# Optimization experiments

Hardware: AMD Instinct MI355X
Metric: run time of the kernel (lower is better)

## Reference

```python
import jax, jax.numpy as jnp
import numpy as np

B, N, C, H = 4, 1024, 768, 12
D = C // H
SCALE = D ** -0.5


def setup_inputs() -> dict:
    key = jax.random.key(0)
    k1, k2, k3, k4 = jax.random.split(key, 4)
    x1 = jax.random.normal(k1, (B, N, C), dtype=jnp.float32)
    x2 = jax.random.normal(k2, (B, N, C), dtype=jnp.float32)
    # shared (dual-stream) Linear2 weights, torch nn.Linear layout: [out, in]
    W_qkv = jax.random.normal(k3, (3 * C, C), dtype=jnp.float32) * (C ** -0.5)
    b_qkv = jnp.zeros((3 * C,), dtype=jnp.float32)
    W_proj = jax.random.normal(k4, (C, C), dtype=jnp.float32) * (C ** -0.5)
    b_proj = jnp.zeros((C,), dtype=jnp.float32)
    return {"x1": x1, "x2": x2, "W_qkv": W_qkv, "b_qkv": b_qkv,
            "W_proj": W_proj, "b_proj": b_proj}


def _split_qkv(x, W_qkv, b_qkv):
    qkv = (x @ W_qkv.T + b_qkv).reshape(B, N, 3, H, D)
    qkv = jnp.transpose(qkv, (2, 0, 3, 1, 4))  # [3,B,H,N,D]
    return qkv[0], qkv[1], qkv[2]


def reference(x1, x2, W_qkv, b_qkv, W_proj, b_proj):
    q1, k1, v1 = _split_qkv(x1, W_qkv, b_qkv)
    q2, k2, v2 = _split_qkv(x2, W_qkv, b_qkv)
    # two score maps, combined before a single shared softmax
    s1 = jnp.einsum("bhqd,bhkd->bhqk", q1 * SCALE, k1)
    s2 = jnp.einsum("bhqd,bhkd->bhqk", q2 * SCALE, k2)
    attn = jax.nn.softmax(s1 + s2, axis=-1)  # [B,H,N,N]
    # same attention matrix applied to both value streams
    o1 = jnp.einsum("bhqk,bhkd->bhqd", attn, v1)
    o2 = jnpum = jnp.einsum("bhqk,bhkd->bhqd", attn, v2) if False else jnp.einsum("bhqk,bhkd->bhqd", attn, v2)
    o1 = jnp.transpose(o1, (0, 2, 1, 3)).reshape(B, N, C)
    o2 = jnp.transpose(o2, (0, 2, 1, 3)).reshape(B, N, C)
    y1 = o1 @ W_proj.T + b_proj
    y2 = o2 @ W_proj.T + b_proj
    return y1, y2
```

## Files before the change

### kernel.cpp

```cpp
#include <hip/hip_runtime.h>
#include <hip/hip_bf16.h>


typedef __bf16 bf16x8 __attribute__((ext_vector_type(8)));
typedef __bf16 bf16x4 __attribute__((ext_vector_type(4)));
typedef float  f32x4  __attribute__((ext_vector_type(4)));

__device__ __forceinline__ bf16x8 cvt8(const float* p) {
    f32x4 f0 = *(const f32x4*)p;
    f32x4 f1 = *(const f32x4*)(p + 4);
    bf16x8 r;
    r[0] = (__bf16)f0[0]; r[1] = (__bf16)f0[1]; r[2] = (__bf16)f0[2]; r[3] = (__bf16)f0[3];
    r[4] = (__bf16)f1[0]; r[5] = (__bf16)f1[1]; r[6] = (__bf16)f1[2]; r[7] = (__bf16)f1[3];
    return r;
}

__device__ __forceinline__ void async16(const __bf16* g, __bf16* l) {
    __builtin_amdgcn_global_load_lds(
        (const __attribute__((address_space(1))) void*)g,
        (__attribute__((address_space(3))) void*)l, 16, 0, 0);
}

__global__ __launch_bounds__(256)
void cvt3_k(const float* __restrict__ x1, const float* __restrict__ x2,
            const float* __restrict__ wq, __bf16* __restrict__ xc,
            __bf16* __restrict__ wqc)
{
    int bid = blockIdx.x;
    const float* src; __bf16* dst; int i;
    if (bid < 1536)      { src = x1; dst = xc;             i = (bid * 256 + threadIdx.x) * 8; }
    else if (bid < 3072) { src = x2; dst = xc + 3145728;   i = ((bid - 1536) * 256 + threadIdx.x) * 8; }
    else                 { src = wq; dst = wqc;            i = ((bid - 3072) * 256 + threadIdx.x) * 8; }
    *(bf16x8*)(dst + i) = cvt8(src + i);
}

__global__ __launch_bounds__(256)
void cvt_k(const float* __restrict__ src, __bf16* __restrict__ dst, int n) {
    int i = (blockIdx.x * 256 + threadIdx.x) * 8;
    if (i < n) *(bf16x8*)(dst + i) = cvt8(src + i);
}

__global__ __launch_bounds__(256)
void gemm_qkv_s(const __bf16* __restrict__ Xc, const __bf16* __restrict__ Wq,
                const float* __restrict__ bias,
                __bf16* __restrict__ qo, __bf16* __restrict__ ko,
                __bf16* __restrict__ vo)
{
    constexpr int K = 768;
    __shared__ __bf16 As[128 * 32];
    __shared__ __bf16 Bs[128 * 32];

    const int t = threadIdx.x, w = t >> 6, lane = t & 63;
    const int l15 = lane & 15, quad = lane >> 4;
    const int wm = w >> 1, wn = w & 1;

    const int bid  = blockIdx.x;
    const int xcd  = bid & 7;
    const int i6   = bid >> 3;
    const int pair = i6 / 18;
    const int gx   = i6 - pair * 18;
    const int p    = xcd * 8 + pair;
    const int gy   = p & 31;
    const int st   = p >> 5;

    const int lrow = lane >> 2, lcol = (lane & 3) * 8;

    const __bf16* Ab = Xc + (size_t)st * 3145728 + (size_t)(gy * 128) * K;
    const __bf16* Bb = Wq + (size_t)(gx * 128) * K;

    f32x4 acc[4][4];
#pragma unroll
    for (int mi = 0; mi < 4; mi++)
#pragma unroll
        for (int ni = 0; ni < 4; ni++) acc[mi][ni] = f32x4{0.f, 0.f, 0.f, 0.f};

    for (int k0 = 0; k0 < K; k0 += 32) {
#pragma unroll
        for (int i = 0; i < 2; i++) {
            int r = w * 32 + i * 16 + lrow;
            async16(Ab + (size_t)r * K + k0 + lcol, &As[r * 32 + lcol]);
            async16(Bb + (size_t)r * K + k0 + lcol, &Bs[r * 32 + lcol]);
        }
        __syncthreads();
        bf16x8 af[4], bfr[4];
#pragma unroll
        for (int mi = 0; mi < 4; mi++)
            af[mi] = *(const bf16x8*)&As[(wm * 64 + mi * 16 + l15) * 32 + quad * 8];
#pragma unroll
        for (int ni = 0; ni < 4; ni++)
            bfr[ni] = *(const bf16x8*)&Bs[(wn * 64 + ni * 16 + l15) * 32 + quad * 8];
#pragma unroll
        for (int mi = 0; mi < 4; mi++)
#pragma unroll
            for (int ni = 0; ni < 4; ni++)
                acc[mi][ni] = __builtin_amdgcn_mfma_f32_16x16x32_bf16(af[mi], bfr[ni], acc[mi][ni], 0, 0, 0);
        __syncthreads();
    }

    const int which = (gx * 128) / 768;

    if (which == 2) {
#pragma unroll
        for (int ni = 0; ni < 4; ni++) {
            int j = gx * 128 + wn * 64 + ni * 16 + l15;
            int c = j - 1536;
            int h = c >> 6, d = c & 63;
            float bj = bias[j];
#pragma unroll
            for (int mi = 0; mi < 4; mi++) {
                int row0 = gy * 128 + wm * 64 + mi * 16 + quad * 4;
                int b = row0 >> 10, tok0 = row0 & 1023;
                bf16x4 pv;
#pragma unroll
                for (int r = 0; r < 4; r++) pv[r] = (__bf16)(acc[mi][ni][r] + bj);
                *(bf16x4*)&vo[((size_t)((st * 4 + b) * 12 + h) * 64 + d) * 1024 + tok0] = pv;
            }
        }
    } else {
#pragma unroll
        for (int ni = 0; ni < 4; ni++) {
            int j     = gx * 128 + wn * 64 + ni * 16 + l15;
            int c     = j - which * 768;
            int h = c >> 6, d = c & 63;
            float bj  = bias[j];
#pragma unroll
            for (int mi = 0; mi < 4; mi++) {
#pragma unroll
                for (int r = 0; r < 4; r++) {
                    int row = gy * 128 + wm * 64 + mi * 16 + quad * 4 + r;
                    int b = row >> 10, tok = row & 1023;
                    float val = acc[mi][ni][r] + bj;
                    if (which == 0)
                        qo[((size_t)((st * 4 + b) * 12 + h) * 1024 + tok) * 64 + d] = (__bf16)(val * 0.125f);
                    else
                        ko[((size_t)((st * 4 + b) * 12 + h) * 1024 + tok) * 64 + d] = (__bf16)val;
                }
            }
        }
    }
}

__global__ __launch_bounds__(256)
void gemm_proj(const __bf16* __restrict__ A, const __bf16* __restrict__ Wp,
               const float* __restrict__ bias, float* __restrict__ out)
{
    constexpr int K = 768;
    __shared__ __bf16 As[128 * 32];
    __shared__ __bf16 Bs[128 * 32];

    const int t = threadIdx.x, w = t >> 6, lane = t & 63;
    const int l15 = lane & 15, quad = lane >> 4;
    const int wm = w >> 1, wn = w & 1;
    const int gx = blockIdx.x, gy = blockIdx.y;
    const int lrow = lane >> 2, lcol = (lane & 3) * 8;

    const __bf16* Ab = A  + (size_t)(gy * 128) * K;
    const __bf16* Bb = Wp + (size_t)(gx * 128) * K;

    f32x4 acc[4][4];
#pragma unroll
    for (int mi = 0; mi < 4; mi++)
#pragma unroll
        for (int ni = 0; ni < 4; ni++) acc[mi][ni] = f32x4{0.f, 0.f, 0.f, 0.f};

    for (int k0 = 0; k0 < K; k0 += 32) {
#pragma unroll
        for (int i = 0; i < 2; i++) {
            int r = w * 32 + i * 16 + lrow;
            async16(Ab + (size_t)r * K + k0 + lcol, &As[r * 32 + lcol]);
            async16(Bb + (size_t)r * K + k0 + lcol, &Bs[r * 32 + lcol]);
        }
        __syncthreads();
        bf16x8 af[4], bfr[4];
#pragma unroll
        for (int mi = 0; mi < 4; mi++)
            af[mi] = *(const bf16x8*)&As[(wm * 64 + mi * 16 + l15) * 32 + quad * 8];
#pragma unroll
        for (int ni = 0; ni < 4; ni++)
            bfr[ni] = *(const bf16x8*)&Bs[(wn * 64 + ni * 16 + l15) * 32 + quad * 8];
#pragma unroll
        for (int mi = 0; mi < 4; mi++)
#pragma unroll
            for (int ni = 0; ni < 4; ni++)
                acc[mi][ni] = __builtin_amdgcn_mfma_f32_16x16x32_bf16(af[mi], bfr[ni], acc[mi][ni], 0, 0, 0);
        __syncthreads();
    }

#pragma unroll
    for (int ni = 0; ni < 4; ni++) {
        int col  = gx * 128 + wn * 64 + ni * 16 + l15;
        float bj = bias[col];
#pragma unroll
        for (int mi = 0; mi < 4; mi++)
#pragma unroll
            for (int r = 0; r < 4; r++) {
                int row = gy * 128 + wm * 64 + mi * 16 + quad * 4 + r;
                out[(size_t)row * 768 + col] = acc[mi][ni][r] + bj;
            }
    }
}

__global__ __launch_bounds__(256)
void attn_k(const __bf16* __restrict__ qws, const __bf16* __restrict__ kws,
            const __bf16* __restrict__ vws, __bf16* __restrict__ ows)
{
    __shared__ __bf16 KV[2][2][2][2][4][512];
    __shared__ __bf16 Ps[4][16 * 72];

    const int g  = blockIdx.x;
    const int qt = g / 48;
    const int bh = g % 48;
    const int b = bh / 12, h = bh % 12;
    const int t = threadIdx.x, w = t >> 6, lane = t & 63;
    const int l15 = lane & 15, quad = lane >> 4;

    const size_t head_off = (size_t)bh * 65536;
    const size_t ss       = (size_t)48 * 65536;

    bf16x8 qf[2][2];
#pragma unroll
    for (int s = 0; s < 2; s++)
#pragma unroll
        for (int kk = 0; kk < 2; kk++)
            qf[s][kk] = *(const bf16x8*)(qws + s * ss + head_off
                          + (size_t)(qt * 64 + w * 16 + l15) * 64 + kk * 32 + quad * 8);

    float lsum = 0.f;
    f32x4 accO[2][4];
#pragma unroll
    for (int s = 0; s < 2; s++)
#pragma unroll
        for (int mi = 0; mi < 4; mi++) accO[s][mi] = f32x4{0.f, 0.f, 0.f, 0.f};

    const int skv = w >> 1, sst = w & 1;
    const __bf16* sbase = (skv ? vws : kws) + head_off + (size_t)sst * ss;

#pragma unroll
    for (int i = 0; i < 8; i++) {
        const int kk = i >> 2, mi = i & 3;
        const __bf16* gp = skv
            ? sbase + (size_t)(mi * 16 + l15) * 1024 + kk * 32 + quad * 8
            : sbase + (size_t)(mi * 16 + l15) * 64 + kk * 32 + quad * 8;
        async16(gp, &KV[0][skv][sst][kk][mi][lane * 8]);
    }
    __syncthreads();

#pragma unroll 2
    for (int kt = 0; kt < 16; kt++) {
        const int cb = kt & 1, nb = cb ^ 1;

        if (kt < 15) {
            const int keyb = (kt + 1) * 64;
#pragma unroll
            for (int i = 0; i < 8; i++) {
                const int kk = i >> 2, mi = i & 3;
                const __bf16* gp = skv
                    ? sbase + (size_t)(mi * 16 + l15) * 1024 + keyb + kk * 32 + quad * 8
                    : sbase + (size_t)(keyb + mi * 16 + l15) * 64 + kk * 32 + quad * 8;
                async16(gp, &KV[nb][skv][sst][kk][mi][lane * 8]);
            }
        }

        f32x4 accS[4];
#pragma unroll
        for (int i = 0; i < 4; i++) accS[i] = f32x4{0.f, 0.f, 0.f, 0.f};
        __builtin_amdgcn_s_setprio(1);
#pragma unroll
        for (int s = 0; s < 2; s++)
#pragma unroll
            for (int kk = 0; kk < 2; kk++) {
                bf16x8 kf[4];
#pragma unroll
                for (int mi = 0; mi < 4; mi++)
                    kf[mi] = *(const bf16x8*)&KV[cb][0][s][kk][mi][lane * 8];
#pragma unroll
                for (int mi = 0; mi < 4; mi++)
                    accS[mi] = __builtin_amdgcn_mfma_f32_16x16x32_bf16(kf[mi], qf[s][kk], accS[mi], 0, 0, 0);
            }
        __builtin_amdgcn_s_setprio(0);

        float rs = 0.f;
        bf16x4 pk[4];
#pragma unroll
        for (int mi = 0; mi < 4; mi++)
#pragma unroll
            for (int r = 0; r < 4; r++) {
                float pv = __expf(accS[mi][r]);
                pk[mi][r] = (__bf16)pv;
                rs += pv;
            }
        lsum += rs;

#pragma unroll
        for (int mi = 0; mi < 4; mi++)
            *(bf16x4*)&Ps[w][l15 * 72 + mi * 16 + quad * 4] = pk[mi];

        __builtin_amdgcn_s_setprio(1);
#pragma unroll
        for (int kk = 0; kk < 2; kk++) {
            bf16x8 pa = *(const bf16x8*)&Ps[w][l15 * 72 + kk * 32 + quad * 8];
#pragma unroll
            for (int s = 0; s < 2; s++)
#pragma unroll
                for (int mi = 0; mi < 4; mi++) {
                    bf16x8 vf = *(const bf16x8*)&KV[cb][1][s][kk][mi][lane * 8];
                    accO[s][mi] = __builtin_amdgcn_mfma_f32_16x16x32_bf16(vf, pa, accO[s][mi], 0, 0, 0);
                }
        }
        __builtin_amdgcn_s_setprio(0);

        __syncthreads();
    }

    lsum += __shfl_xor(lsum, 16);
    lsum += __shfl_xor(lsum, 32);
    float il = 1.f / lsum;

    const int tok = qt * 64 + w * 16 + l15;
#pragma unroll
    for (int s = 0; s < 2; s++)
#pragma unroll
        for (int mi = 0; mi < 4; mi++) {
            bf16x4 ov;
#pragma unroll
            for (int r = 0; r < 4; r++) ov[r] = (__bf16)(accO[s][mi][r] * il);
            *(bf16x4*)&ows[((size_t)((s * 4 + b) * 1024 + tok)) * 768
                           + h * 64 + mi * 16 + quad * 4] = ov;
        }
}

extern "C" void kernel_launch(void* const* d_in, const int* in_sizes, int n_in,
                              void* d_out, int out_size, void* d_ws, size_t ws_size,
                              hipStream_t stream)
{
    const float* x1    = (const float*)d_in[0];
    const float* x2    = (const float*)d_in[1];
    const float* Wqkv  = (const float*)d_in[2];
    const float* bqkv  = (const float*)d_in[3];
    const float* Wproj = (const float*)d_in[4];
    const float* bproj = (const float*)d_in[5];
    float* out = (float*)d_out;

    const size_t qkv_elems = (size_t)2 * 4 * 12 * 1024 * 64;
    __bf16* q_ws = (__bf16*)d_ws;
    __bf16* k_ws = q_ws + qkv_elems;
    __bf16* v_ws = k_ws + qkv_elems;
    __bf16* pool = v_ws + qkv_elems;
    __bf16* Wqc  = pool + 3145728;
    __bf16* o_ws = pool;
    __bf16* Wpc  = q_ws;
    __bf16* Xc   = (__bf16*)d_out;

    cvt3_k<<<3936, 256, 0, stream>>>(x1, x2, Wqkv, Xc, Wqc);
    gemm_qkv_s<<<1152, 256, 0, stream>>>(Xc, Wqc, bqkv, q_ws, k_ws, v_ws);
    attn_k<<<768, 256, 0, stream>>>(q_ws, k_ws, v_ws, o_ws);
    cvt_k<<<288, 256, 0, stream>>>(Wproj, Wpc, 589824);
    gemm_proj<<<dim3(6, 64), 256, 0, stream>>>(o_ws, Wpc, bproj, out);
}
```

Measured before the change: 228.3 us.

## Restructure attention to two waves each handling 32 queries with smaller key tiles

New measurement: 219.1 us. 1.04x faster.

```diff
diff --git a/kernel.cpp b/kernel.cpp
--- a/kernel.cpp
+++ b/kernel.cpp
@@ -200,12 +200,13 @@
     }
 }
 
-__global__ __launch_bounds__(256)
+__global__ __launch_bounds__(128, 2)
 void attn_k(const __bf16* __restrict__ qws, const __bf16* __restrict__ kws,
             const __bf16* __restrict__ vws, __bf16* __restrict__ ows)
 {
-    __shared__ __bf16 KV[2][2][2][2][4][512];
-    __shared__ __bf16 Ps[4][16 * 72];
+    __shared__ __bf16 Ks[2][2][2][2][512];
+    __shared__ __bf16 Vs[2][2][4][512];
+    __shared__ __bf16 Ps[2][2][16 * 72];
 
     const int g  = blockIdx.x;
     const int qt = g / 48;
@@ -217,116 +218,131 @@
     const size_t head_off = (size_t)bh * 65536;
     const size_t ss       = (size_t)48 * 65536;
 
-    bf16x8 qf[2][2];
-#pragma unroll
-    for (int s = 0; s < 2; s++)
-#pragma unroll
-        for (int kk = 0; kk < 2; kk++)
-            qf[s][kk] = *(const bf16x8*)(qws + s * ss + head_off
-                          + (size_t)(qt * 64 + w * 16 + l15) * 64 + kk * 32 + quad * 8);
-
-    float lsum = 0.f;
-    f32x4 accO[2][4];
-#pragma unroll
-    for (int s = 0; s < 2; s++)
-#pragma unroll
-        for (int mi = 0; mi < 4; mi++) accO[s][mi] = f32x4{0.f, 0.f, 0.f, 0.f};
-
-    const int skv = w >> 1, sst = w & 1;
-    const __bf16* sbase = (skv ? vws : kws) + head_off + (size_t)sst * ss;
-
-#pragma unroll
-    for (int i = 0; i < 8; i++) {
-        const int kk = i >> 2, mi = i & 3;
-        const __bf16* gp = skv
-            ? sbase + (size_t)(mi * 16 + l15) * 1024 + kk * 32 + quad * 8
-            : sbase + (size_t)(mi * 16 + l15) * 64 + kk * 32 + quad * 8;
-        async16(gp, &KV[0][skv][sst][kk][mi][lane * 8]);
-    }
+    bf16x8 qf[2][2][2];
+#pragma unroll
+    for (int set = 0; set < 2; set++)
+#pragma unroll
+        for (int s = 0; s < 2; s++)
+#pragma unroll
+            for (int kk = 0; kk < 2; kk++)
+                qf[set][s][kk] = *(const bf16x8*)(qws + s * ss + head_off
+                    + (size_t)(qt * 64 + w * 32 + set * 16 + l15) * 64 + kk * 32 + quad * 8);
+
+    float lsum[2] = {0.f, 0.f};
+    f32x4 accO[2][2][4];
+#pragma unroll
+    for (int set = 0; set < 2; set++)
+#pragma unroll
+        for (int s = 0; s < 2; s++)
+#pragma unroll
+            for (int mi = 0; mi < 4; mi++) accO[set][s][mi] = f32x4{0.f, 0.f, 0.f, 0.f};
+
+    const __bf16* kbase = kws + head_off;
+    const __bf16* vbase = vws + head_off;
+
+#define STAGE_TILE(BUF, KEYB)                                                   \
+    do {                                                                        \
+        if (w == 0) {                                                           \
+            _Pragma("unroll")                                                   \
+            for (int i = 0; i < 8; i++) {                                       \
+                const int s = i >> 2, kk = (i >> 1) & 1, mi = i & 1;            \
+                async16(kbase + s * ss + (size_t)((KEYB) + mi * 16 + l15) * 64  \
+                            + kk * 32 + quad * 8,                               \
+                        &Ks[BUF][s][kk][mi][lane * 8]);                         \
+            }                                                                   \
+        } else {                                                                \
+            _Pragma("unroll")                                                   \
+            for (int i = 0; i < 8; i++) {                                       \
+                const int s = i >> 2, mi = i & 3;                               \
+                async16(vbase + s * ss + (size_t)(mi * 16 + l15) * 1024         \
+                            + (KEYB) + quad * 8,                                \
+                        &Vs[BUF][s][mi][lane * 8]);                             \
+            }                                                                   \
+        }                                                                       \
+    } while (0)
+
+    STAGE_TILE(0, 0);
     __syncthreads();
 
 #pragma unroll 2
-    for (int kt = 0; kt < 16; kt++) {
+    for (int kt = 0; kt < 32; kt++) {
         const int cb = kt & 1, nb = cb ^ 1;
 
-        if (kt < 15) {
-            const int keyb = (kt + 1) * 64;
-#pragma unroll
-            for (int i = 0; i < 8; i++) {
-                const int kk = i >> 2, mi = i & 3;
-                const __bf16* gp = skv
-                    ? sbase + (size_t)(mi * 16 + l15) * 1024 + keyb + kk * 32 + quad * 8
-                    : sbase + (size_t)(keyb + mi * 16 + l15) * 64 + kk * 32 + quad * 8;
-                async16(gp, &KV[nb][skv][sst][kk][mi][lane * 8]);
-            }
-        }
-
-        f32x4 accS[4];
-#pragma unroll
-        for (int i = 0; i < 4; i++) accS[i] = f32x4{0.f, 0.f, 0.f, 0.f};
+        if (kt < 31) STAGE_TILE(nb, (kt + 1) * 32);
+
+        f32x4 accS[2][2];
+#pragma unroll
+        for (int set = 0; set < 2; set++)
+#pragma unroll
+            for (int mi = 0; mi < 2; mi++) accS[set][mi] = f32x4{0.f, 0.f, 0.f, 0.f};
         __builtin_amdgcn_s_setprio(1);
 #pragma unroll
         for (int s = 0; s < 2; s++)
 #pragma unroll
             for (int kk = 0; kk < 2; kk++) {
-                bf16x8 kf[4];
-#pragma unroll
-                for (int mi = 0; mi < 4; mi++)
-                    kf[mi] = *(const bf16x8*)&KV[cb][0][s][kk][mi][lane * 8];
-#pragma unroll
-                for (int mi = 0; mi < 4; mi++)
-                    accS[mi] = __builtin_amdgcn_mfma_f32_16x16x32_bf16(kf[mi], qf[s][kk], accS[mi], 0, 0, 0);
+                bf16x8 kf0 = *(const bf16x8*)&Ks[cb][s][kk][0][lane * 8];
+                bf16x8 kf1 = *(const bf16x8*)&Ks[cb][s][kk][1][lane * 8];
+#pragma unroll
+                for (int set = 0; set < 2; set++) {
+                    accS[set][0] = __builtin_amdgcn_mfma_f32_16x16x32_bf16(kf0, qf[set][s][kk], accS[set][0], 0, 0, 0);
+                    accS[set][1] = __builtin_amdgcn_mfma_f32_16x16x32_bf16(kf1, qf[set][s][kk], accS[set][1], 0, 0, 0);
+                }
             }
         __builtin_amdgcn_s_setprio(0);
 
-        float rs = 0.f;
-        bf16x4 pk[4];
-#pragma unroll
-        for (int mi = 0; mi < 4; mi++)
-#pragma unroll
-            for (int r = 0; r < 4; r++) {
-                float pv = __expf(accS[mi][r]);
-                pk[mi][r] = (__bf16)pv;
-                rs += pv;
-            }
-        lsum += rs;
-
-#pragma unroll
-        for (int mi = 0; mi < 4; mi++)
-            *(bf16x4*)&Ps[w][l15 * 72 + mi * 16 + quad * 4] = pk[mi];
-
+#pragma unroll
+        for (int set = 0; set < 2; set++) {
+            float rs = 0.f;
+#pragma unroll
+            for (int mi = 0; mi < 2; mi++) {
+                bf16x4 pk;
+#pragma unroll
+                for (int r = 0; r < 4; r++) {
+                    float pv = __expf(accS[set][mi][r]);
+                    pk[r] = (__bf16)pv;
+                    rs += pv;
+                }
+                *(bf16x4*)&Ps[w][set][l15 * 72 + mi * 16 + quad * 4] = pk;
+            }
+            lsum[set] += rs;
+        }
+
+        bf16x8 pa0 = *(const bf16x8*)&Ps[w][0][l15 * 72 + quad * 8];
+        bf16x8 pa1 = *(const bf16x8*)&Ps[w][1][l15 * 72 + quad * 8];
         __builtin_amdgcn_s_setprio(1);
 #pragma unroll
-        for (int kk = 0; kk < 2; kk++) {
-            bf16x8 pa = *(const bf16x8*)&Ps[w][l15 * 72 + kk * 32 + quad * 8];
-#pragma unroll
-            for (int s = 0; s < 2; s++)
-#pragma unroll
-                for (int mi = 0; mi < 4; mi++) {
-                    bf16x8 vf = *(const bf16x8*)&KV[cb][1][s][kk][mi][lane * 8];
-                    accO[s][mi] = __builtin_amdgcn_mfma_f32_16x16x32_bf16(vf, pa, accO[s][mi], 0, 0, 0);
-                }
-        }
+        for (int s = 0; s < 2; s++)
+#pragma unroll
+            for (int mi = 0; mi < 4; mi++) {
+                bf16x8 vf = *(const bf16x8*)&Vs[cb][s][mi][lane * 8];
+                accO[0][s][mi] = __builtin_amdgcn_mfma_f32_16x16x32_bf16(vf, pa0, accO[0][s][mi], 0, 0, 0);
+                accO[1][s][mi] = __builtin_amdgcn_mfma_f32_16x16x32_bf16(vf, pa1, accO[1][s][mi], 0, 0, 0);
+            }
         __builtin_amdgcn_s_setprio(0);
 
         __syncthreads();
     }
-
-    lsum += __shfl_xor(lsum, 16);
-    lsum += __shfl_xor(lsum, 32);
-    float il = 1.f / lsum;
-
-    const int tok = qt * 64 + w * 16 + l15;
-#pragma unroll
-    for (int s = 0; s < 2; s++)
-#pragma unroll
-        for (int mi = 0; mi < 4; mi++) {
-            bf16x4 ov;
-#pragma unroll
-            for (int r = 0; r < 4; r++) ov[r] = (__bf16)(accO[s][mi][r] * il);
-            *(bf16x4*)&ows[((size_t)((s * 4 + b) * 1024 + tok)) * 768
-                           + h * 64 + mi * 16 + quad * 4] = ov;
-        }
+#undef STAGE_TILE
+
+#pragma unroll
+    for (int set = 0; set < 2; set++) {
+        float l = lsum[set];
+        l += __shfl_xor(l, 16);
+        l += __shfl_xor(l, 32);
+        float il = 1.f / l;
+
+        const int tok = qt * 64 + w * 32 + set * 16 + l15;
+#pragma unroll
+        for (int s = 0; s < 2; s++)
+#pragma unroll
+            for (int mi = 0; mi < 4; mi++) {
+                bf16x4 ov;
+#pragma unroll
+                for (int r = 0; r < 4; r++) ov[r] = (__bf16)(accO[set][s][mi][r] * il);
+                *(bf16x4*)&ows[((size_t)((s * 4 + b) * 1024 + tok)) * 768
+                               + h * 64 + mi * 16 + quad * 4] = ov;
+            }
+    }
 }
 
 extern "C" void kernel_launch(void* const* d_in, const int* in_sizes, int n_in,
@@ -353,7 +369,7 @@
 
     cvt3_k<<<3936, 256, 0, stream>>>(x1, x2, Wqkv, Xc, Wqc);
     gemm_qkv_s<<<1152, 256, 0, stream>>>(Xc, Wqc, bqkv, q_ws, k_ws, v_ws);
-    attn_k<<<768, 256, 0, stream>>>(q_ws, k_ws, v_ws, o_ws);
+    attn_k<<<768, 128, 0, stream>>>(q_ws, k_ws, v_ws, o_ws);
     cvt_k<<<288, 256, 0, stream>>>(Wproj, Wpc, 589824);
     gemm_proj<<<dim3(6, 64), 256, 0, stream>>>(o_ws, Wpc, bproj, out);
 }
```
